# Optimization experiments

Measured on AMD Instinct MI355X. Metric: run time of the kernel, lower is better.

Reference implementation:

```python
import jax, jax.numpy as jnp
import numpy as np

N_NODES = 50000
N_EDGES = 1600000
D = 64


def setup_inputs() -> dict:
    key = jax.random.key(0)
    ks = jax.random.split(key, 7)
    scale = 1.0 / np.sqrt(2 * D)  # keep activations sane through relu stack
    x = jax.random.normal(ks[0], (N_NODES, D), dtype=jnp.float32)
    edge_index = jax.random.randint(ks[1], (2, N_EDGES), 0, N_NODES, dtype=jnp.int32)
    edge_weight = jax.random.uniform(ks[2], (N_EDGES,), dtype=jnp.float32)
    W1 = jax.random.normal(ks[3], (D, 2 * D), dtype=jnp.float32) * scale
    b1 = jax.random.normal(ks[4], (D,), dtype=jnp.float32) * 0.01
    W2 = jax.random.normal(ks[5], (D, 2 * D), dtype=jnp.float32) * scale
    b2 = jax.random.normal(ks[6], (D,), dtype=jnp.float32) * 0.01
    return {"x": x, "edge_index": edge_index, "edge_weight": edge_weight,
            "W1": W1, "b1": b1, "W2": W2, "b2": b2}


def _sage_conv(x, src, dst, edge_weight, W, b):
    # gather neighbor features, weight, scatter-mean onto src nodes
    m = x[dst] * edge_weight[:, None]                      # [E, d]
    agg_sum = jax.ops.segment_sum(m, src, num_segments=x.shape[0])
    cnt = jax.ops.segment_sum(jnp.ones_like(edge_weight), src,
                              num_segments=x.shape[0])
    agg = agg_sum / jnp.maximum(cnt, 1.0)[:, None]          # scatter 'mean'
    h = jnp.concatenate([x, agg], axis=1)                   # [N, 2d]
    return h @ W.T + b


def reference(x, edge_index, edge_weight, W1, b1, W2, b2):
    src, dst = edge_index[0], edge_index[1]
    h = jax.nn.relu(_sage_conv(x, src, dst, edge_weight, W1, b1))
    h = jax.nn.relu(_sage_conv(h, src, dst, edge_weight, W2, b2))
    return h
```

## Files before the change

kernel.cpp:

```cpp
#include <hip/hip_runtime.h>

#define NN 50000
#define NE 1600000
#define DD 64
#define NPB 196
#define NBKT 256
#define CHUNK 2500
#define NBLK 640
#define SLOT 24
#define SSTR 25
#define S1CAP 1024
#define SPCAP 512
#define ELLW 80

typedef __attribute__((ext_vector_type(8))) short bf16x8;
typedef __attribute__((ext_vector_type(4))) float f32x4;
typedef __attribute__((ext_vector_type(2))) float f32x2;

static __device__ __forceinline__ unsigned short f2bf(float f) {
    unsigned int u = __float_as_uint(f);
    unsigned int r = (u + 0x7FFFu + ((u >> 16) & 1u)) >> 16;
    return (unsigned short)r;
}
static __device__ __forceinline__ float bf2f(unsigned short h) {
    return __uint_as_float((unsigned int)h << 16);
}
static __device__ __forceinline__ unsigned int pk_fp8x4(float a, float b, float c, float d) {
    unsigned int p = __builtin_amdgcn_cvt_pk_fp8_f32(a, b, 0u, false);
    p = __builtin_amdgcn_cvt_pk_fp8_f32(c, d, p, true);
    return p;
}

__global__ __launch_bounds__(256) void prep_bin(
    const int* __restrict__ ei, const float* __restrict__ ew,
    int* __restrict__ gcur, int* __restrict__ gspillc,
    int2* __restrict__ buf1, int2* __restrict__ spill,
    const float* __restrict__ x, ushort* __restrict__ xb,
    unsigned int* __restrict__ xf8,
    const float* __restrict__ W1, const float* __restrict__ W2,
    ushort* __restrict__ W1b, ushort* __restrict__ W2b)
{
    __shared__ int2 slot[NBKT * SSTR];
    __shared__ int  lcnt[NBKT];
    __shared__ int  lbase[NBKT];
    int tid = threadIdx.x;
    int blk = blockIdx.x;

    if (blk >= NBLK) {
        int pb = blk - NBLK;
        if (pb < 3125) {
            int i = pb * 256 + tid;
            float4 v = ((const float4*)x)[i];
            ushort4 o;
            o.x = f2bf(v.x); o.y = f2bf(v.y); o.z = f2bf(v.z); o.w = f2bf(v.w);
            ((ushort4*)xb)[i] = o;
            xf8[i] = pk_fp8x4(v.x, v.y, v.z, v.w);
        } else {
            int i = (pb - 3125) * 256 + tid;
            const float* src = (i < 2048) ? W1 : W2;
            ushort* dst = (i < 2048) ? W1b : W2b;
            int j = i & 2047;
            float4 v = ((const float4*)src)[j];
            ushort4 o;
            o.x = f2bf(v.x); o.y = f2bf(v.y); o.z = f2bf(v.z); o.w = f2bf(v.w);
            ((ushort4*)dst)[j] = o;
        }
        return;
    }

    int shard = blk & 7;
    for (int b = tid; b < NBKT; b += 256) lcnt[b] = 0;
    __syncthreads();

    int g0 = blk * (CHUNK / 4);
    const int4*   s4 = (const int4*)ei;
    const int4*   d4 = ((const int4*)ei) + NE / 4;
    const float4* w4 = (const float4*)ew;
    for (int it = 0; it < 3; ++it) {
        int idx = it * 256 + tid;
        if (idx >= CHUNK / 4) break;
        int4 sv = s4[g0 + idx];
        int4 dv = d4[g0 + idx];
        float4 wv = w4[g0 + idx];
#pragma unroll
        for (int k = 0; k < 4; ++k) {
            int s = (k == 0) ? sv.x : (k == 1) ? sv.y : (k == 2) ? sv.z : sv.w;
            int d = (k == 0) ? dv.x : (k == 1) ? dv.y : (k == 2) ? dv.z : dv.w;
            float w = (k == 0) ? wv.x : (k == 1) ? wv.y : (k == 2) ? wv.z : wv.w;
            int bkt = s / NPB;
            int sloc = s - bkt * NPB;
            int2 rec = make_int2(d | ((int)f2bf(w) << 16), sloc);
            int pos = atomicAdd(&lcnt[bkt], 1);
            if (pos < SLOT) {
                slot[bkt * SSTR + pos] = rec;
            } else {
                int sp = atomicAdd(&gspillc[bkt], 1);
                if (sp < SPCAP) spill[bkt * SPCAP + sp] = rec;
            }
        }
    }
    __syncthreads();

    {
        int b = tid;
        int n = lcnt[b]; if (n > SLOT) n = SLOT;
        lcnt[b] = n;
        lbase[b] = (n > 0) ? atomicAdd(&gcur[b * 8 + shard], n) : 0;
    }
    __syncthreads();

    int wave = tid >> 6, lane = tid & 63;
    int b0 = wave * 64;
    int vcnt = lcnt[b0 + lane];
    int vbase = lbase[b0 + lane];
#pragma unroll 8
    for (int j = 0; j < 64; ++j) {
        int n = __shfl(vcnt, j);
        int base = __shfl(vbase, j);
        int b = b0 + j;
        if (lane < n) {
            int2 rec = slot[b * SSTR + lane];
            int p = base + lane;
            if (p < S1CAP) {
                buf1[((size_t)b * 8 + shard) * S1CAP + p] = rec;
            } else {
                int sp = atomicAdd(&gspillc[b], 1);
                if (sp < SPCAP) spill[b * SPCAP + sp] = rec;
            }
        }
    }
}

__global__ __launch_bounds__(1024) void build_ell(
    const int* __restrict__ gcur, const int2* __restrict__ buf1,
    const int* __restrict__ gspillc, const int2* __restrict__ spill,
    unsigned int* __restrict__ csr, int* __restrict__ cnt)
{
    __shared__ int cur[NPB];
    int tid = threadIdx.x, bkt = blockIdx.x;

    if (tid < NPB) cur[tid] = 0;
    __syncthreads();

    for (int sh = 0; sh < 9; ++sh) {
        int n; const int2* rp;
        if (sh < 8) {
            n = gcur[bkt * 8 + sh]; if (n > S1CAP) n = S1CAP;
            rp = buf1 + ((size_t)bkt * 8 + sh) * S1CAP;
        } else {
            n = gspillc[bkt]; if (n > SPCAP) n = SPCAP;
            rp = spill + (size_t)bkt * SPCAP;
        }
        for (int i = tid; i < n; i += 1024) {
            int2 r = rp[i];
            int pos = atomicAdd(&cur[r.y], 1);
            if (pos < ELLW)
                csr[((size_t)(bkt * NPB + r.y)) * ELLW + pos] = (unsigned int)r.x;
        }
    }
    __syncthreads();

    if (tid < NPB) {
        int node = bkt * NPB + tid;
        if (node < NN) {
            int deg = cur[tid];
            cnt[node] = deg;
            int c = deg < ELLW ? deg : ELLW;
            int c16 = (c + 15) & ~15;
            for (int p = c; p < c16; ++p)
                csr[(size_t)node * ELLW + p] = 0u;
        }
    }
}

__global__ __launch_bounds__(512) void fused_layer(
    const ushort* __restrict__ Xb,
    const unsigned int* __restrict__ f8,
    const int* __restrict__ cnt, const unsigned int* __restrict__ csr,
    const ushort* __restrict__ Wb, const float* __restrict__ bias,
    float* __restrict__ out, ushort* __restrict__ outb,
    unsigned char* __restrict__ outf8)
{
    __shared__ ushort xL[16][72];
    __shared__ ushort aggL[16][72];
    int tid = threadIdx.x;
    int wave = tid >> 6, lane = tid & 63;
    int g = lane >> 4, l16 = lane & 15;
    int base = blockIdx.x * 16;
    int nodeA = base + wave;
    int nodeB = base + wave + 8;

    if (lane < 16) {
        *(ushort4*)&xL[wave][l16 * 4] =
            *(const ushort4*)&Xb[(size_t)nodeA * DD + l16 * 4];
        *(ushort4*)&xL[wave + 8][l16 * 4] =
            *(const ushort4*)&Xb[(size_t)nodeB * DD + l16 * 4];
    }

    int ndA = cnt[nodeA], ndB = cnt[nodeB];
    int nA = ndA < ELLW ? ndA : ELLW;
    int nB = ndB < ELLW ? ndB : ELLW;
    int nA16 = (nA + 15) & ~15;
    int nB16 = (nB + 15) & ~15;
    int imax = nA16 > nB16 ? nA16 : nB16;
    const unsigned int* __restrict__ rpA = csr + (size_t)nodeA * ELLW;
    const unsigned int* __restrict__ rpB = csr + (size_t)nodeB * ELLW;
    float aA0 = 0.f, aA1 = 0.f, aA2 = 0.f, aA3 = 0.f;
    float aB0 = 0.f, aB1 = 0.f, aB2 = 0.f, aB3 = 0.f;

    for (int i = 0; i < imax; i += 16) {
        uint4 rA, rB;
        bool doA = i < nA16, doB = i < nB16;
        if (doA) rA = *(const uint4*)(rpA + i + g * 4);
        if (doB) rB = *(const uint4*)(rpB + i + g * 4);
        if (doA) {
            unsigned int v0 = f8[(rA.x & 0xFFFF) * 16 + l16];
            unsigned int v1 = f8[(rA.y & 0xFFFF) * 16 + l16];
            unsigned int v2 = f8[(rA.z & 0xFFFF) * 16 + l16];
            unsigned int v3 = f8[(rA.w & 0xFFFF) * 16 + l16];
            float w0 = bf2f((unsigned short)(rA.x >> 16));
            float w1 = bf2f((unsigned short)(rA.y >> 16));
            float w2 = bf2f((unsigned short)(rA.z >> 16));
            float w3 = bf2f((unsigned short)(rA.w >> 16));
            f32x2 lo, hi;
            lo = __builtin_amdgcn_cvt_pk_f32_fp8(v0, false);
            hi = __builtin_amdgcn_cvt_pk_f32_fp8(v0, true);
            aA0 += w0 * lo.x; aA1 += w0 * lo.y; aA2 += w0 * hi.x; aA3 += w0 * hi.y;
            lo = __builtin_amdgcn_cvt_pk_f32_fp8(v1, false);
            hi = __builtin_amdgcn_cvt_pk_f32_fp8(v1, true);
            aA0 += w1 * lo.x; aA1 += w1 * lo.y; aA2 += w1 * hi.x; aA3 += w1 * hi.y;
            lo = __builtin_amdgcn_cvt_pk_f32_fp8(v2, false);
            hi = __builtin_amdgcn_cvt_pk_f32_fp8(v2, true);
            aA0 += w2 * lo.x; aA1 += w2 * lo.y; aA2 += w2 * hi.x; aA3 += w2 * hi.y;
            lo = __builtin_amdgcn_cvt_pk_f32_fp8(v3, false);
            hi = __builtin_amdgcn_cvt_pk_f32_fp8(v3, true);
            aA0 += w3 * lo.x; aA1 += w3 * lo.y; aA2 += w3 * hi.x; aA3 += w3 * hi.y;
        }
        if (doB) {
            unsigned int v0 = f8[(rB.x & 0xFFFF) * 16 + l16];
            unsigned int v1 = f8[(rB.y & 0xFFFF) * 16 + l16];
            unsigned int v2 = f8[(rB.z & 0xFFFF) * 16 + l16];
            unsigned int v3 = f8[(rB.w & 0xFFFF) * 16 + l16];
            float w0 = bf2f((unsigned short)(rB.x >> 16));
            float w1 = bf2f((unsigned short)(rB.y >> 16));
            float w2 = bf2f((unsigned short)(rB.z >> 16));
            float w3 = bf2f((unsigned short)(rB.w >> 16));
            f32x2 lo, hi;
            lo = __builtin_amdgcn_cvt_pk_f32_fp8(v0, false);
            hi = __builtin_amdgcn_cvt_pk_f32_fp8(v0, true);
            aB0 += w0 * lo.x; aB1 += w0 * lo.y; aB2 += w0 * hi.x; aB3 += w0 * hi.y;
            lo = __builtin_amdgcn_cvt_pk_f32_fp8(v1, false);
            hi = __builtin_amdgcn_cvt_pk_f32_fp8(v1, true);
            aB0 += w1 * lo.x; aB1 += w1 * lo.y; aB2 += w1 * hi.x; aB3 += w1 * hi.y;
            lo = __builtin_amdgcn_cvt_pk_f32_fp8(v2, false);
            hi = __builtin_amdgcn_cvt_pk_f32_fp8(v2, true);
            aB0 += w2 * lo.x; aB1 += w2 * lo.y; aB2 += w2 * hi.x; aB3 += w2 * hi.y;
            lo = __builtin_amdgcn_cvt_pk_f32_fp8(v3, false);
            hi = __builtin_amdgcn_cvt_pk_f32_fp8(v3, true);
            aB0 += w3 * lo.x; aB1 += w3 * lo.y; aB2 += w3 * hi.x; aB3 += w3 * hi.y;
        }
    }

    aA0 += __shfl_xor(aA0, 16); aA0 += __shfl_xor(aA0, 32);
    aA1 += __shfl_xor(aA1, 16); aA1 += __shfl_xor(aA1, 32);
    aA2 += __shfl_xor(aA2, 16); aA2 += __shfl_xor(aA2, 32);
    aA3 += __shfl_xor(aA3, 16); aA3 += __shfl_xor(aA3, 32);
    aB0 += __shfl_xor(aB0, 16); aB0 += __shfl_xor(aB0, 32);
    aB1 += __shfl_xor(aB1, 16); aB1 += __shfl_xor(aB1, 32);
    aB2 += __shfl_xor(aB2, 16); aB2 += __shfl_xor(aB2, 32);
    aB3 += __shfl_xor(aB3, 16); aB3 += __shfl_xor(aB3, 32);

    if (lane < 16) {
        float dmA = (float)(ndA > 1 ? ndA : 1);
        float dmB = (float)(ndB > 1 ? ndB : 1);
        ushort4 oA, oB;
        oA.x = f2bf(aA0 / dmA); oA.y = f2bf(aA1 / dmA);
        oA.z = f2bf(aA2 / dmA); oA.w = f2bf(aA3 / dmA);
        oB.x = f2bf(aB0 / dmB); oB.y = f2bf(aB1 / dmB);
        oB.z = f2bf(aB2 / dmB); oB.w = f2bf(aB3 / dmB);
        *(ushort4*)&aggL[wave][l16 * 4] = oA;
        *(ushort4*)&aggL[wave + 8][l16 * 4] = oB;
    }
    __syncthreads();

    if (wave < 4) {
        f32x4 acc = (f32x4){0.f, 0.f, 0.f, 0.f};
#pragma unroll
        for (int ki = 0; ki < 4; ++ki) {
            const ushort* ap = (ki < 2) ? &xL[l16][ki * 32 + g * 8]
                                        : &aggL[l16][(ki - 2) * 32 + g * 8];
            bf16x8 af = *(const bf16x8*)ap;
            bf16x8 bfrag = *(const bf16x8*)&Wb[(size_t)(wave * 16 + l16) * 128 + ki * 32 + g * 8];
            acc = __builtin_amdgcn_mfma_f32_16x16x32_bf16(af, bfrag, acc, 0, 0, 0);
        }
        int col = wave * 16 + l16;
        float bv = bias[col];
#pragma unroll
        for (int r = 0; r < 4; ++r) {
            int grow = base + g * 4 + r;
            float v = fmaxf(acc[r] + bv, 0.f);
            if (out)  out[(size_t)grow * DD + col] = v;
            if (outb) outb[(size_t)grow * DD + col] = f2bf(v);
            if (outf8) {
                unsigned int p = __builtin_amdgcn_cvt_pk_fp8_f32(v, v, 0u, false);
                outf8[(size_t)grow * DD + col] = (unsigned char)(p & 0xFFu);
            }
        }
    }
}

extern "C" void kernel_launch(void* const* d_in, const int* in_sizes, int n_in,
                              void* d_out, int out_size, void* d_ws, size_t ws_size,
                              hipStream_t stream)
{
    const float* x  = (const float*)d_in[0];
    const int*   ei = (const int*)d_in[1];
    const float* ew = (const float*)d_in[2];
    const float* W1 = (const float*)d_in[3];
    const float* b1 = (const float*)d_in[4];
    const float* W2 = (const float*)d_in[5];
    const float* b2 = (const float*)d_in[6];
    float* out = (float*)d_out;

    char* ws = (char*)d_ws;
    int*          gcur    = (int*)ws;
    int*          gspillc = (int*)(ws + 8192);
    int2*         buf1    = (int2*)(ws + 16384);
    int2*         spill   = (int2*)(ws + 16793600);
    unsigned int* csr     = (unsigned int*)(ws + 17842176);
    int*          cnt     = (int*)(ws + 33898496);
    ushort*       xb      = (ushort*)(ws + 34099200);
    ushort*       h1b     = (ushort*)(ws + 40499200);
    ushort*       W1b     = (ushort*)(ws + 46899200);
    ushort*       W2b     = (ushort*)(ws + 46915584);
    unsigned int* xf8     = (unsigned int*)(ws + 46931968);
    unsigned char* h1f8   = (unsigned char*)(ws + 50131968);

    hipMemsetAsync(gcur, 0, 9216, stream);

    prep_bin<<<NBLK + 3141, 256, 0, stream>>>(ei, ew, gcur, gspillc, buf1, spill,
                                              x, xb, xf8, W1, W2, W1b, W2b);
    build_ell<<<NBKT, 1024, 0, stream>>>(gcur, buf1, gspillc, spill, csr, cnt);

    fused_layer<<<NN / 16, 512, 0, stream>>>(xb, xf8, cnt, csr, W1b, b1,
                                             nullptr, h1b, h1f8);
    fused_layer<<<NN / 16, 512, 0, stream>>>(h1b, (const unsigned int*)h1f8,
                                             cnt, csr, W2b, b2, out, nullptr, nullptr);
}
```

Before: 174.2 us.

## Split ELL build into half-bucket blocks and widen prep_bin flush writes

build_ell now launches two blocks per bucket, each owning half of the bucket's nodes. Each block reads every record in the bucket but only inserts those in its half, and the eight shards are processed by eight thread groups in parallel. The point is to double block-level parallelism (256 blocks is about one per CU) and cut shared-atomic contention, at the cost of reading each bucket twice. prep_bin's flush loop also handles four buckets per wave iteration with 16 lanes each, instead of one bucket per iteration with up to 24 active lanes, to improve lane utilisation.

```diff
diff --git a/kernel.cpp b/kernel.cpp
--- a/kernel.cpp
+++ b/kernel.cpp
@@ -4,6 +4,7 @@
 #define NE 1600000
 #define DD 64
 #define NPB 196
+#define HPB 98
 #define NBKT 256
 #define CHUNK 2500
 #define NBLK 640
@@ -110,23 +111,26 @@
     __syncthreads();
 
     int wave = tid >> 6, lane = tid & 63;
-    int b0 = wave * 64;
-    int vcnt = lcnt[b0 + lane];
-    int vbase = lbase[b0 + lane];
-#pragma unroll 8
-    for (int j = 0; j < 64; ++j) {
-        int n = __shfl(vcnt, j);
-        int base = __shfl(vbase, j);
-        int b = b0 + j;
-        if (lane < n) {
-            int2 rec = slot[b * SSTR + lane];
-            int p = base + lane;
-            if (p < S1CAP) {
-                buf1[((size_t)b * 8 + shard) * S1CAP + p] = rec;
-            } else {
-                int sp = atomicAdd(&gspillc[b], 1);
-                if (sp < SPCAP) spill[b * SPCAP + sp] = rec;
-            }
+    int grp = lane >> 4, l16 = lane & 15;
+#pragma unroll 4
+    for (int jj = 0; jj < 16; ++jj) {
+        int b = wave * 64 + jj * 4 + grp;
+        int n = lcnt[b];
+        int base = lbase[b];
+        int2* dst = &buf1[((size_t)b * 8 + shard) * S1CAP];
+        if (l16 < n) {
+            int2 rec = slot[b * SSTR + l16];
+            int p = base + l16;
+            if (p < S1CAP) dst[p] = rec;
+            else { int sp = atomicAdd(&gspillc[b], 1);
+                   if (sp < SPCAP) spill[b * SPCAP + sp] = rec; }
+        }
+        if (l16 + 16 < n) {
+            int2 rec = slot[b * SSTR + l16 + 16];
+            int p = base + l16 + 16;
+            if (p < S1CAP) dst[p] = rec;
+            else { int sp = atomicAdd(&gspillc[b], 1);
+                   if (sp < SPCAP) spill[b * SPCAP + sp] = rec; }
         }
     }
 }
@@ -136,32 +140,52 @@
     const int* __restrict__ gspillc, const int2* __restrict__ spill,
     unsigned int* __restrict__ csr, int* __restrict__ cnt)
 {
-    __shared__ int cur[NPB];
-    int tid = threadIdx.x, bkt = blockIdx.x;
-
-    if (tid < NPB) cur[tid] = 0;
-    __syncthreads();
-
-    for (int sh = 0; sh < 9; ++sh) {
-        int n; const int2* rp;
-        if (sh < 8) {
-            n = gcur[bkt * 8 + sh]; if (n > S1CAP) n = S1CAP;
-            rp = buf1 + ((size_t)bkt * 8 + sh) * S1CAP;
-        } else {
-            n = gspillc[bkt]; if (n > SPCAP) n = SPCAP;
-            rp = spill + (size_t)bkt * SPCAP;
-        }
+    __shared__ int cur[HPB];
+    __shared__ int cnts[9];
+    int tid = threadIdx.x;
+    int bkt  = blockIdx.x >> 1;
+    int nlo  = (blockIdx.x & 1) * HPB;
+
+    if (tid < HPB) cur[tid] = 0;
+    if (tid >= 128 && tid < 137) {
+        int sh = tid - 128;
+        int n = (sh < 8) ? gcur[bkt * 8 + sh] : gspillc[bkt];
+        int cap = (sh < 8) ? S1CAP : SPCAP;
+        cnts[sh] = n < cap ? n : cap;
+    }
+    __syncthreads();
+
+    {
+        int sh = tid >> 7, lt = tid & 127;
+        int n = cnts[sh];
+        const int2* rp = buf1 + ((size_t)bkt * 8 + sh) * S1CAP;
+        for (int i = lt; i < n; i += 128) {
+            int2 r = rp[i];
+            int node = r.y - nlo;
+            if ((unsigned)node < HPB) {
+                int pos = atomicAdd(&cur[node], 1);
+                if (pos < ELLW)
+                    csr[((size_t)(bkt * NPB + r.y)) * ELLW + pos] = (unsigned int)r.x;
+            }
+        }
+    }
+    {
+        int n = cnts[8];
+        const int2* rp = spill + (size_t)bkt * SPCAP;
         for (int i = tid; i < n; i += 1024) {
             int2 r = rp[i];
-            int pos = atomicAdd(&cur[r.y], 1);
-            if (pos < ELLW)
-                csr[((size_t)(bkt * NPB + r.y)) * ELLW + pos] = (unsigned int)r.x;
-        }
-    }
-    __syncthreads();
-
-    if (tid < NPB) {
-        int node = bkt * NPB + tid;
+            int node = r.y - nlo;
+            if ((unsigned)node < HPB) {
+                int pos = atomicAdd(&cur[node], 1);
+                if (pos < ELLW)
+                    csr[((size_t)(bkt * NPB + r.y)) * ELLW + pos] = (unsigned int)r.x;
+            }
+        }
+    }
+    __syncthreads();
+
+    if (tid < HPB) {
+        int node = bkt * NPB + nlo + tid;
         if (node < NN) {
             int deg = cur[tid];
             cnt[node] = deg;
@@ -340,7 +364,7 @@
 
     prep_bin<<<NBLK + 3141, 256, 0, stream>>>(ei, ew, gcur, gspillc, buf1, spill,
                                               x, xb, xf8, W1, W2, W1b, W2b);
-    build_ell<<<NBKT, 1024, 0, stream>>>(gcur, buf1, gspillc, spill, csr, cnt);
+    build_ell<<<NBKT * 2, 1024, 0, stream>>>(gcur, buf1, gspillc, spill, csr, cnt);
 
     fused_layer<<<NN / 16, 512, 0, stream>>>(xb, xf8, cnt, csr, W1b, b1,
                                              nullptr, h1b, h1f8);
```

Result: no change. 174.7 us (+0.2%).
